# Kernel tuning notes

Hardware: AMD Instinct MI355X
Metric: run time of the kernel (lower is better)

## Reference

```python
import jax, jax.numpy as jnp
import numpy as np

N, T, D_FEAT, H = 8192, 60, 6, 64
NEG_SLOPE = 0.01  # torch LeakyReLU default


def setup_inputs() -> dict:
    key = jax.random.key(0)
    ks = jax.random.split(key, 20)
    s = lambda k, shape, fan: jax.random.normal(k, shape, jnp.float32) * (1.0 / np.sqrt(fan))
    inp = {
        'x': jax.random.normal(ks[0], (N, T, D_FEAT), jnp.float32),
        # LSTM layer 0 (input D_FEAT) and layer 1 (input H); gate order i,f,g,o
        'Wih0': s(ks[1], (4 * H, D_FEAT), H), 'Whh0': s(ks[2], (4 * H, H), H),
        'bih0': s(ks[3], (4 * H,), H), 'bhh0': s(ks[4], (4 * H,), H),
        'Wih1': s(ks[5], (4 * H, H), H), 'Whh1': s(ks[6], (4 * H, H), H),
        'bih1': s(ks[7], (4 * H,), H), 'bhh1': s(ks[8], (4 * H,), H),
        # GAT layer: transformation Linear(H,H) and attention vector a [2H,1] (randn in torch)
        'Wt': s(ks[9], (H, H), H), 'bt': s(ks[10], (H,), H),
        'a': jax.random.normal(ks[11], (2 * H, 1), jnp.float32),
        # fc and fc_out
        'Wfc': s(ks[12], (H, H), H), 'bfc': s(ks[13], (H,), H),
        'Wout': s(ks[14], (1, H), H), 'bout': s(ks[15], (1,), H),
    }
    return inp


def _lstm_layer(x, Wih, Whh, bih, bhh):
    # x: [N, T, Din] -> outputs [N, T, H]
    xg = jnp.einsum('ntd,gd->ntg', x, Wih) + bih + bhh  # precompute input gates

    def step(carry, xt):
        h, c = carry
        gates = xt + h @ Whh.T  # [N, 4H]
        i, f, g, o = jnp.split(gates, 4, axis=-1)
        c = jax.nn.sigmoid(f) * c + jax.nn.sigmoid(i) * jnp.tanh(g)
        h = jax.nn.sigmoid(o) * jnp.tanh(c)
        return (h, c), h

    n = x.shape[0]
    h0 = jnp.zeros((n, Whh.shape[1]), x.dtype)
    (_, _), hs = jax.lax.scan(step, (h0, h0), jnp.swapaxes(xg, 0, 1))
    return jnp.swapaxes(hs, 0, 1)


def _gat_layer(x, Wt, bt, a):
    # att[i,j] = leaky_relu(a1 . Wx_j + a2 . Wx_i); softmax over j; out = att @ x
    h = x @ Wt.T + bt                    # [N, H]
    hdim = h.shape[1]
    s1 = (h @ a[:hdim]).squeeze(-1)      # a1 . Wx_j  -> column term
    s2 = (h @ a[hdim:]).squeeze(-1)      # a2 . Wx_i  -> row term
    scores = jax.nn.leaky_relu(s2[:, None] + s1[None, :], NEG_SLOPE)  # [N, N]
    att = jax.nn.softmax(scores, axis=1)
    return att @ x


def reference(x, Wih0, Whh0, bih0, bhh0, Wih1, Whh1, bih1, bhh1,
              Wt, bt, a, Wfc, bfc, Wout, bout):
    out = _lstm_layer(x, Wih0, Whh0, bih0, bhh0)
    out = _lstm_layer(out, Wih1, Whh1, bih1, bhh1)
    last = out[:, -1, :]                 # [N, H]
    hidden = _gat_layer(last, Wt, bt, a) + last  # num_layers_gat = 1
    hidden = jax.nn.leaky_relu(hidden @ Wfc.T + bfc, NEG_SLOPE)
    return (hidden @ Wout.T + bout).squeeze(-1)  # [N]
```

## Files before the change

kernel.cpp:

```cpp
#include <hip/hip_runtime.h>

#define NN 8192
#define TT 60
#define DF 6
#define HH 64
#define GG 256
#define RS 132
#define CH 128
#define NCH (NN / CH)

typedef _Float16 half8 __attribute__((ext_vector_type(8)));
typedef float f32x4 __attribute__((ext_vector_type(4)));
#define MFMA16(a, b, c) __builtin_amdgcn_mfma_f32_16x16x32_f16((a), (b), (c), 0, 0, 0)

__device__ __forceinline__ float sigmoidf_(float x) {
    return __builtin_amdgcn_rcpf(1.0f + __expf(-x));
}
__device__ __forceinline__ float tanhf_(float x) {
    return __builtin_fmaf(2.0f, __builtin_amdgcn_rcpf(1.0f + __expf(-2.0f * x)), -1.0f);
}
__device__ __forceinline__ float lrelu_(float x) { return x > 0.0f ? x : 0.01f * x; }

__device__ __forceinline__ half8 ldw8(const float* __restrict__ p) {
    const float4* q = (const float4*)p;
    float4 u = q[0], v = q[1];
    half8 r;
    r[0]=(_Float16)u.x; r[1]=(_Float16)u.y; r[2]=(_Float16)u.z; r[3]=(_Float16)u.w;
    r[4]=(_Float16)v.x; r[5]=(_Float16)v.y; r[6]=(_Float16)v.z; r[7]=(_Float16)v.w;
    return r;
}

#define SXW (TT * 8 + 8)

__global__ __launch_bounds__(256, 2)
void lstm_fused_kernel(const float* __restrict__ x,
                       const float* __restrict__ Wih0, const float* __restrict__ Whh0,
                       const float* __restrict__ bih0, const float* __restrict__ bhh0,
                       const float* __restrict__ Wih1, const float* __restrict__ Whh1,
                       const float* __restrict__ bih1, const float* __restrict__ bhh1,
                       float* __restrict__ last_out)
{
    __shared__ _Float16 sxp[16][SXW];
    __shared__ _Float16 h0buf[2][16][72];
    __shared__ _Float16 h1buf[2][16][72];
    __shared__ _Float16 zero16[8];

    const int tid  = threadIdx.x;
    const int w    = tid >> 6;
    const int lane = tid & 63;
    const int quad = lane >> 4;
    const int l15  = lane & 15;
    const int hc   = w * 16 + l15;
    const int n0   = blockIdx.x * 16;

    for (int i = tid; i < 16 * SXW / 2; i += 256) ((unsigned*)sxp)[i] = 0u;
    for (int i = tid; i < 2 * 16 * 72 / 2; i += 256) ((unsigned*)h0buf)[i] = 0u;
    for (int i = tid; i < 2 * 16 * 72 / 2; i += 256) ((unsigned*)h1buf)[i] = 0u;
    if (tid < 4) ((unsigned*)zero16)[tid] = 0u;
    __syncthreads();

    for (int idx = tid; idx < 16 * TT * DF; idx += 256) {
        const int m = idx / (TT * DF);
        const int r = idx - m * (TT * DF);
        const int t = r / DF;
        const int d = r - t * DF;
        sxp[m][t * 8 + d] = (_Float16)x[(size_t)(n0 + m) * (TT * DF) + r];
    }

    half8 bhh0f[4][2], bih1f[4][2], bhh1f[4][2], bxf[4];
    float bias0[4], bias1[4];
    #pragma unroll
    for (int nt = 0; nt < 4; nt++) {
        const int g = nt * 64 + hc;
        #pragma unroll
        for (int kc = 0; kc < 2; kc++) {
            const int k0 = kc * 32 + quad * 8;
            bhh0f[nt][kc] = ldw8(Whh0 + (size_t)g * HH + k0);
            bih1f[nt][kc] = ldw8(Wih1 + (size_t)g * HH + k0);
            bhh1f[nt][kc] = ldw8(Whh1 + (size_t)g * HH + k0);
        }
        bias0[nt] = bih0[g] + bhh0[g];
        bias1[nt] = bih1[g] + bhh1[g];
        half8 t;
        #pragma unroll
        for (int j = 0; j < 8; j++) t[j] = (_Float16)0.f;
        if (quad == 0) {
            #pragma unroll
            for (int j = 0; j < DF; j++) t[j] = (_Float16)Wih0[g * DF + j];
        }
        bxf[nt] = t;
    }

    float c0[4] = {0.f, 0.f, 0.f, 0.f};
    float c1[4] = {0.f, 0.f, 0.f, 0.f};
    __syncthreads();

    int p = 0;
    for (int t = 0; t < TT; t++) {
        const half8 a_h0_0 = *(const half8*)&h0buf[p][l15][quad * 8];
        const half8 a_h0_1 = *(const half8*)&h0buf[p][l15][32 + quad * 8];
        const half8 a_h1_0 = *(const half8*)&h1buf[p][l15][quad * 8];
        const half8 a_h1_1 = *(const half8*)&h1buf[p][l15][32 + quad * 8];
        const _Float16* xap = (quad == 0) ? &sxp[l15][t * 8] : zero16;
        const half8 ax = *(const half8*)xap;

        f32x4 g0v[4];
        #pragma unroll
        for (int nt = 0; nt < 4; nt++) {
            f32x4 c; c[0] = bias0[nt]; c[1] = bias0[nt]; c[2] = bias0[nt]; c[3] = bias0[nt];
            c = MFMA16(ax, bxf[nt], c);
            c = MFMA16(a_h0_0, bhh0f[nt][0], c);
            c = MFMA16(a_h0_1, bhh0f[nt][1], c);
            g0v[nt] = c;
        }
        _Float16 (*h0w)[72] = h0buf[p ^ 1];
        #pragma unroll
        for (int reg = 0; reg < 4; reg++) {
            const float gi = g0v[0][reg], gf = g0v[1][reg], gc = g0v[2][reg], go = g0v[3][reg];
            const float cc = sigmoidf_(gf) * c0[reg] + sigmoidf_(gi) * tanhf_(gc);
            c0[reg] = cc;
            h0w[quad * 4 + reg][hc] = (_Float16)(sigmoidf_(go) * tanhf_(cc));
        }
        __syncthreads();

        const half8 a_h0n_0 = *(const half8*)&h0buf[p ^ 1][l15][quad * 8];
        const half8 a_h0n_1 = *(const half8*)&h0buf[p ^ 1][l15][32 + quad * 8];
        f32x4 g1v[4];
        #pragma unroll
        for (int nt = 0; nt < 4; nt++) {
            f32x4 c; c[0] = bias1[nt]; c[1] = bias1[nt]; c[2] = bias1[nt]; c[3] = bias1[nt];
            c = MFMA16(a_h0n_0, bih1f[nt][0], c);
            c = MFMA16(a_h0n_1, bih1f[nt][1], c);
            c = MFMA16(a_h1_0, bhh1f[nt][0], c);
            c = MFMA16(a_h1_1, bhh1f[nt][1], c);
            g1v[nt] = c;
        }
        _Float16 (*h1w)[72] = h1buf[p ^ 1];
        #pragma unroll
        for (int reg = 0; reg < 4; reg++) {
            const float gi = g1v[0][reg], gf = g1v[1][reg], gc = g1v[2][reg], go = g1v[3][reg];
            const float cc = sigmoidf_(gf) * c1[reg] + sigmoidf_(gi) * tanhf_(gc);
            c1[reg] = cc;
            const float hv = sigmoidf_(go) * tanhf_(cc);
            h1w[quad * 4 + reg][hc] = (_Float16)hv;
            if (t == TT - 1) last_out[(size_t)(n0 + quad * 4 + reg) * HH + hc] = hv;
        }
        __syncthreads();
        p ^= 1;
    }
}

__global__ void gat_prep_kernel(const float* __restrict__ last,
                                const float* __restrict__ Wt, const float* __restrict__ bt,
                                const float* __restrict__ a,
                                float* __restrict__ s1, float* __restrict__ s2,
                                float* __restrict__ blkmax)
{
    __shared__ float sWtT[HH][HH + 1];
    __shared__ float slast[16][HH];
    __shared__ float sbt[HH], sa1[HH], sa2[HH];
    __shared__ float swm[4];
    const int tid = threadIdx.x;
    for (int idx = tid; idx < HH * HH; idx += 256) {
        const int h = idx >> 6, d = idx & 63;
        sWtT[d][h] = Wt[idx];
    }
    if (tid < HH) { sbt[tid] = bt[tid]; sa1[tid] = a[tid]; sa2[tid] = a[HH + tid]; }
    const int n0 = blockIdx.x * 16;
    for (int idx = tid; idx < 16 * HH; idx += 256)
        (&slast[0][0])[idx] = last[(size_t)n0 * HH + idx];
    __syncthreads();
    const int w = tid >> 6, l = tid & 63;
    float wmax = -1e30f;
    for (int rr = 0; rr < 4; rr++) {
        const int r = w * 4 + rr;
        float acc = sbt[l];
        #pragma unroll
        for (int d = 0; d < HH; d++) acc += slast[r][d] * sWtT[d][l];
        float p1 = acc * sa1[l], p2 = acc * sa2[l];
        #pragma unroll
        for (int off = 32; off > 0; off >>= 1) {
            p1 += __shfl_xor(p1, off);
            p2 += __shfl_xor(p2, off);
        }
        if (l == 0) { s1[n0 + r] = p1; s2[n0 + r] = p2; }
        wmax = fmaxf(wmax, p1);
    }
    if (l == 0) swm[w] = wmax;
    __syncthreads();
    if (tid == 0) blkmax[blockIdx.x] = fmaxf(fmaxf(swm[0], swm[1]), fmaxf(swm[2], swm[3]));
}

__global__ void gat_finalize_kernel(const float* __restrict__ s1, const float* __restrict__ s2,
                                    const float* __restrict__ blkmax,
                                    float* __restrict__ Z, float* __restrict__ Ai, float* __restrict__ Bi,
                                    float* __restrict__ Dj, float* __restrict__ Uj, float* __restrict__ Wj,
                                    int* __restrict__ rank)
{
    __shared__ float red[256];
    const int tid = threadIdx.x;
    red[tid] = fmaxf(blkmax[tid], blkmax[tid + 256]);
    __syncthreads();
    for (int s = 128; s > 0; s >>= 1) {
        if (tid < s) red[tid] = fmaxf(red[tid], red[tid + s]);
        __syncthreads();
    }
    const float s1max = red[0];
    for (int i = blockIdx.x * 256 + tid; i < NN; i += 256 * 32) {
        const float z  = s2[i] + s1max;
        const float mi = lrelu_(z);
        Z[i]  = z;
        Ai[i] = __expf(z - mi);
        Bi[i] = __expf(0.01f * z - mi);
        const float d = s1[i] - s1max;
        Dj[i] = d;
        Uj[i] = __expf(d);
        Wj[i] = __expf(0.01f * d);
        rank[i] = 0;
    }
}

__global__ __launch_bounds__(256)
void rank_kernel(const float* __restrict__ Dj, int* __restrict__ rank)
{
    __shared__ float sd[1024];
    const int tid = threadIdx.x;
    const int j   = blockIdx.x * 256 + tid;
    const float dj = Dj[j];
    const int kbase = blockIdx.y * 1024;
    for (int i = tid; i < 1024; i += 256) sd[i] = Dj[kbase + i];
    __syncthreads();
    int cnt = 0;
    #pragma unroll 4
    for (int q = 0; q < 256; q++) {
        const float4 dk = ((const float4*)sd)[q];
        const int k0 = kbase + q * 4;
        cnt += (dk.x < dj || (dk.x == dj && k0     < j)) ? 1 : 0;
        cnt += (dk.y < dj || (dk.y == dj && k0 + 1 < j)) ? 1 : 0;
        cnt += (dk.z < dj || (dk.z == dj && k0 + 2 < j)) ? 1 : 0;
        cnt += (dk.w < dj || (dk.w == dj && k0 + 3 < j)) ? 1 : 0;
    }
    atomicAdd(&rank[j], cnt);
}

__global__ __launch_bounds__(256)
void scatter_kernel(const float* __restrict__ last,
                    const float* __restrict__ Dj, const float* __restrict__ Uj,
                    const float* __restrict__ Wj, const int* __restrict__ rank,
                    float* __restrict__ sortedRow, float* __restrict__ sortedD)
{
    const int tid = threadIdx.x;
    const int wv = tid >> 6, lane = tid & 63;
    #pragma unroll
    for (int it = 0; it < 8; it++) {
        const int j = blockIdx.x * 32 + wv * 8 + it;
        const int r = rank[j];
        const float u = Uj[j], w = Wj[j];
        const float lv = last[(size_t)j * HH + lane];
        float* row = sortedRow + (size_t)r * RS;
        row[lane]      = u * lv;
        row[64 + lane] = w * lv;
        if (lane == 0) {
            row[128] = u;
            row[129] = w;
            sortedD[r] = Dj[j];
        }
    }
}

__global__ __launch_bounds__(256)
void scanA_kernel(const float* __restrict__ sortedRow, float* __restrict__ chunkSum)
{
    const int c = threadIdx.x;
    if (c >= 130) return;
    const int b = blockIdx.x;
    const float* base = sortedRow + (size_t)b * CH * RS + c;
    float s = 0.f;
    #pragma unroll 8
    for (int r = 0; r < CH; r++) s += base[(size_t)r * RS];
    chunkSum[b * RS + c] = s;
}

__global__ __launch_bounds__(256)
void scanB_kernel(const float* __restrict__ chunkSum, float* __restrict__ chunkOfs)
{
    const int c = threadIdx.x;
    if (c >= 130) return;
    const bool rev = (c < 64) || (c == 128);
    float run = 0.f;
    if (rev) {
        for (int b = NCH - 1; b >= 0; b--) { chunkOfs[b * RS + c] = run; run += chunkSum[b * RS + c]; }
    } else {
        for (int b = 0; b < NCH; b++)      { chunkOfs[b * RS + c] = run; run += chunkSum[b * RS + c]; }
    }
}

__global__ __launch_bounds__(256)
void scanC_kernel(const float* __restrict__ sortedRow, const float* __restrict__ chunkOfs,
                  float* __restrict__ PP)
{
    const int c = threadIdx.x;
    if (c >= 130) return;
    const int b = blockIdx.x;
    const bool rev = (c < 64) || (c == 128);
    float run = chunkOfs[b * RS + c];
    if (rev) {
        if (b == NCH - 1) PP[(size_t)NN * RS + c] = 0.f;
        for (int r = CH - 1; r >= 0; r--) {
            const size_t t = (size_t)b * CH + r;
            run += sortedRow[t * RS + c];
            PP[t * RS + c] = run;
        }
    } else {
        for (int r = 0; r < CH; r++) {
            const size_t t = (size_t)b * CH + r;
            PP[t * RS + c] = run;
            run += sortedRow[t * RS + c];
        }
        if (b == NCH - 1) PP[(size_t)NN * RS + c] = run;
    }
}

__global__ __launch_bounds__(256)
void apply_kernel(const float* __restrict__ last,
                  const float* __restrict__ Z, const float* __restrict__ Ai, const float* __restrict__ Bi,
                  const float* __restrict__ sortedD, const float* __restrict__ PP,
                  float* __restrict__ gout)
{
    const int tid = threadIdx.x;
    const int wv = tid >> 6, lane = tid & 63;
    const int base_i = (blockIdx.x * 4 + wv) * 8;
    for (int batch = 0; batch < 2; batch++) {
        const int i0 = base_i + batch * 4;
        float zi[4]; int lo[4], hi[4];
        #pragma unroll
        for (int q = 0; q < 4; q++) { zi[q] = Z[i0 + q]; lo[q] = 0; hi[q] = NN; }
        for (int iter = 0; iter < 13; iter++) {
            #pragma unroll
            for (int q = 0; q < 4; q++) {
                if (lo[q] < hi[q]) {
                    const int mid = (lo[q] + hi[q]) >> 1;
                    const float dm = sortedD[mid];
                    if (zi[q] + dm > 0.f) hi[q] = mid; else lo[q] = mid + 1;
                }
            }
        }
        #pragma unroll
        for (int q = 0; q < 4; q++) {
            const int i = i0 + q;
            const int t = lo[q];
            const float ai = Ai[i], bi = Bi[i];
            const float* row = PP + (size_t)t * RS;
            const float pu  = row[lane];
            const float pw  = row[64 + lane];
            const float pud = row[128];
            const float pwd = row[129];
            const float numer = bi * pw + ai * pu;
            const float den   = bi * pwd + ai * pud;
            const float lv = last[(size_t)i * HH + lane];
            gout[(size_t)i * HH + lane] = numer * __builtin_amdgcn_rcpf(den) + lv;
        }
    }
}

__global__ void fc_out_kernel(const float* __restrict__ gout,
                              const float* __restrict__ Wfc, const float* __restrict__ bfc,
                              const float* __restrict__ Wout, const float* __restrict__ bout,
                              float* __restrict__ out)
{
    __shared__ float sW[HH][HH + 1];
    __shared__ float sb[HH], sa[HH];
    const int tid = threadIdx.x;
    for (int idx = tid; idx < HH * HH; idx += 256) {
        const int h = idx >> 6, d = idx & 63;
        sW[d][h] = Wfc[idx];
    }
    if (tid < HH) { sb[tid] = bfc[tid]; sa[tid] = Wout[tid]; }
    __syncthreads();
    const int w = tid >> 6, l = tid & 63;
    const float bo = bout[0];
    int n = blockIdx.x * 8 + w * 2;
    for (int rep = 0; rep < 2; rep++, n++) {
        const float vl = gout[(size_t)n * HH + l];
        float acc = sb[l];
        #pragma unroll
        for (int d = 0; d < HH; d++) acc += __shfl(vl, d) * sW[d][l];
        float prod = lrelu_(acc) * sa[l];
        #pragma unroll
        for (int off = 32; off > 0; off >>= 1) prod += __shfl_xor(prod, off);
        if (l == 0) out[n] = prod + bo;
    }
}

extern "C" void kernel_launch(void* const* d_in, const int* in_sizes, int n_in,
                              void* d_out, int out_size, void* d_ws, size_t ws_size,
                              hipStream_t stream)
{
    (void)in_sizes; (void)n_in; (void)out_size; (void)ws_size;
    const float* x    = (const float*)d_in[0];
    const float* Wih0 = (const float*)d_in[1];
    const float* Whh0 = (const float*)d_in[2];
    const float* bih0 = (const float*)d_in[3];
    const float* bhh0 = (const float*)d_in[4];
    const float* Wih1 = (const float*)d_in[5];
    const float* Whh1 = (const float*)d_in[6];
    const float* bih1 = (const float*)d_in[7];
    const float* bhh1 = (const float*)d_in[8];
    const float* Wt   = (const float*)d_in[9];
    const float* bt   = (const float*)d_in[10];
    const float* a    = (const float*)d_in[11];
    const float* Wfc  = (const float*)d_in[12];
    const float* bfc  = (const float*)d_in[13];
    const float* Wout = (const float*)d_in[14];
    const float* bout = (const float*)d_in[15];
    float* out = (float*)d_out;

    float* ws        = (float*)d_ws;
    float* last      = ws;
    float* gout      = last + (size_t)NN*HH;
    float* s1        = gout + (size_t)NN*HH;
    float* s2        = s1 + NN;
    float* Z         = s2 + NN;
    float* Ai        = Z + NN;
    float* Bi        = Ai + NN;
    float* Dj        = Bi + NN;
    float* Uj        = Dj + NN;
    float* Wj        = Uj + NN;
    float* blkmax    = Wj + NN;
    int*   rank      = (int*)(blkmax + 512);
    float* sortedD   = (float*)(rank + NN);
    float* sortedRow = sortedD + NN;
    float* PP        = sortedRow + (size_t)NN*RS;
    float* chunkSum  = PP + (size_t)(NN+1)*RS;
    float* chunkOfs  = chunkSum + NCH*RS;

    lstm_fused_kernel<<<dim3(NN / 16), dim3(256), 0, stream>>>(
        x, Wih0, Whh0, bih0, bhh0, Wih1, Whh1, bih1, bhh1, last);
    gat_prep_kernel<<<dim3(NN / 16), dim3(256), 0, stream>>>(
        last, Wt, bt, a, s1, s2, blkmax);
    gat_finalize_kernel<<<dim3(32), dim3(256), 0, stream>>>(
        s1, s2, blkmax, Z, Ai, Bi, Dj, Uj, Wj, rank);
    rank_kernel<<<dim3(NN / 256, 8), dim3(256), 0, stream>>>(Dj, rank);
    scatter_kernel<<<dim3(NN / 32), dim3(256), 0, stream>>>(
        last, Dj, Uj, Wj, rank, sortedRow, sortedD);
    scanA_kernel<<<dim3(NCH), dim3(256), 0, stream>>>(sortedRow, chunkSum);
    scanB_kernel<<<dim3(1), dim3(256), 0, stream>>>(chunkSum, chunkOfs);
    scanC_kernel<<<dim3(NCH), dim3(256), 0, stream>>>(sortedRow, chunkOfs, PP);
    apply_kernel<<<dim3(NN / 32), dim3(256), 0, stream>>>(
        last, Z, Ai, Bi, sortedD, PP, gout);
    fc_out_kernel<<<dim3(NN / 8), dim3(256), 0, stream>>>(
        gout, Wfc, bfc, Wout, bout, out);
}
```

Before: 287.9 us.

## Pipeline LSTM layers across wave groups, fold chunk offsets into scan, fuse apply+fc

The LSTM kernel now uses 512 threads, split into two wave groups. Layer 0 computes step i while layer 1 computes step i-1 in the same iteration, which halves the barriers per timestep and lets the two layers' MFMA work overlap. The single-block scanB kernel is removed; each scanC block now recomputes its own chunk offset by summing chunkSum directly. The apply and fc_out kernels are fused, so the gout intermediate is no longer written and reread. In exchange, the LSTM block is larger and each scanC block does redundant offset reads.

```diff
diff --git a/kernel.cpp b/kernel.cpp
--- a/kernel.cpp
+++ b/kernel.cpp
@@ -32,7 +32,7 @@
 
 #define SXW (TT * 8 + 8)
 
-__global__ __launch_bounds__(256, 2)
+__global__ __launch_bounds__(512, 4)
 void lstm_fused_kernel(const float* __restrict__ x,
                        const float* __restrict__ Wih0, const float* __restrict__ Whh0,
                        const float* __restrict__ bih0, const float* __restrict__ bhh0,
@@ -47,19 +47,21 @@
 
     const int tid  = threadIdx.x;
     const int w    = tid >> 6;
+    const int grp  = w >> 2;
+    const int cg   = w & 3;
     const int lane = tid & 63;
     const int quad = lane >> 4;
     const int l15  = lane & 15;
-    const int hc   = w * 16 + l15;
+    const int hc   = cg * 16 + l15;
     const int n0   = blockIdx.x * 16;
 
-    for (int i = tid; i < 16 * SXW / 2; i += 256) ((unsigned*)sxp)[i] = 0u;
-    for (int i = tid; i < 2 * 16 * 72 / 2; i += 256) ((unsigned*)h0buf)[i] = 0u;
-    for (int i = tid; i < 2 * 16 * 72 / 2; i += 256) ((unsigned*)h1buf)[i] = 0u;
+    for (int i = tid; i < 16 * SXW / 2; i += 512) ((unsigned*)sxp)[i] = 0u;
+    for (int i = tid; i < 2 * 16 * 72 / 2; i += 512) ((unsigned*)h0buf)[i] = 0u;
+    for (int i = tid; i < 2 * 16 * 72 / 2; i += 512) ((unsigned*)h1buf)[i] = 0u;
     if (tid < 4) ((unsigned*)zero16)[tid] = 0u;
     __syncthreads();
 
-    for (int idx = tid; idx < 16 * TT * DF; idx += 256) {
+    for (int idx = tid; idx < 16 * TT * DF; idx += 512) {
         const int m = idx / (TT * DF);
         const int r = idx - m * (TT * DF);
         const int t = r / DF;
@@ -67,86 +69,97 @@
         sxp[m][t * 8 + d] = (_Float16)x[(size_t)(n0 + m) * (TT * DF) + r];
     }
 
-    half8 bhh0f[4][2], bih1f[4][2], bhh1f[4][2], bxf[4];
-    float bias0[4], bias1[4];
+    half8 wA[4][2], wB[4][2];
+    float bias[4];
+    half8 hzero;
     #pragma unroll
-    for (int nt = 0; nt < 4; nt++) {
-        const int g = nt * 64 + hc;
-        #pragma unroll
-        for (int kc = 0; kc < 2; kc++) {
-            const int k0 = kc * 32 + quad * 8;
-            bhh0f[nt][kc] = ldw8(Whh0 + (size_t)g * HH + k0);
-            bih1f[nt][kc] = ldw8(Wih1 + (size_t)g * HH + k0);
-            bhh1f[nt][kc] = ldw8(Whh1 + (size_t)g * HH + k0);
-        }
-        bias0[nt] = bih0[g] + bhh0[g];
-        bias1[nt] = bih1[g] + bhh1[g];
-        half8 t;
-        #pragma unroll
-        for (int j = 0; j < 8; j++) t[j] = (_Float16)0.f;
-        if (quad == 0) {
-            #pragma unroll
-            for (int j = 0; j < DF; j++) t[j] = (_Float16)Wih0[g * DF + j];
-        }
-        bxf[nt] = t;
-    }
-
-    float c0[4] = {0.f, 0.f, 0.f, 0.f};
-    float c1[4] = {0.f, 0.f, 0.f, 0.f};
-    __syncthreads();
-
-    int p = 0;
-    for (int t = 0; t < TT; t++) {
-        const half8 a_h0_0 = *(const half8*)&h0buf[p][l15][quad * 8];
-        const half8 a_h0_1 = *(const half8*)&h0buf[p][l15][32 + quad * 8];
-        const half8 a_h1_0 = *(const half8*)&h1buf[p][l15][quad * 8];
-        const half8 a_h1_1 = *(const half8*)&h1buf[p][l15][32 + quad * 8];
-        const _Float16* xap = (quad == 0) ? &sxp[l15][t * 8] : zero16;
-        const half8 ax = *(const half8*)xap;
-
-        f32x4 g0v[4];
+    for (int j = 0; j < 8; j++) hzero[j] = (_Float16)0.f;
+
+    if (grp == 0) {
         #pragma unroll
         for (int nt = 0; nt < 4; nt++) {
-            f32x4 c; c[0] = bias0[nt]; c[1] = bias0[nt]; c[2] = bias0[nt]; c[3] = bias0[nt];
-            c = MFMA16(ax, bxf[nt], c);
-            c = MFMA16(a_h0_0, bhh0f[nt][0], c);
-            c = MFMA16(a_h0_1, bhh0f[nt][1], c);
-            g0v[nt] = c;
-        }
-        _Float16 (*h0w)[72] = h0buf[p ^ 1];
-        #pragma unroll
-        for (int reg = 0; reg < 4; reg++) {
-            const float gi = g0v[0][reg], gf = g0v[1][reg], gc = g0v[2][reg], go = g0v[3][reg];
-            const float cc = sigmoidf_(gf) * c0[reg] + sigmoidf_(gi) * tanhf_(gc);
-            c0[reg] = cc;
-            h0w[quad * 4 + reg][hc] = (_Float16)(sigmoidf_(go) * tanhf_(cc));
+            const int g = nt * 64 + hc;
+            wA[nt][0] = ldw8(Whh0 + (size_t)g * HH + quad * 8);
+            wA[nt][1] = ldw8(Whh0 + (size_t)g * HH + 32 + quad * 8);
+            bias[nt]  = bih0[g] + bhh0[g];
+            half8 t = hzero;
+            if (quad == 0) {
+                #pragma unroll
+                for (int j = 0; j < DF; j++) t[j] = (_Float16)Wih0[g * DF + j];
+            }
+            wB[nt][0] = t;
+            wB[nt][1] = hzero;
+        }
+    } else {
+        #pragma unroll
+        for (int nt = 0; nt < 4; nt++) {
+            const int g = nt * 64 + hc;
+            wA[nt][0] = ldw8(Wih1 + (size_t)g * HH + quad * 8);
+            wA[nt][1] = ldw8(Wih1 + (size_t)g * HH + 32 + quad * 8);
+            wB[nt][0] = ldw8(Whh1 + (size_t)g * HH + quad * 8);
+            wB[nt][1] = ldw8(Whh1 + (size_t)g * HH + 32 + quad * 8);
+            bias[nt]  = bih1[g] + bhh1[g];
+        }
+    }
+
+    float cs[4] = {0.f, 0.f, 0.f, 0.f};
+    __syncthreads();
+
+    for (int i = 0; i <= TT; i++) {
+        const int p = i & 1;
+        if (grp == 0) {
+            if (i < TT) {
+                const half8 a0 = *(const half8*)&h0buf[p][l15][quad * 8];
+                const half8 a1 = *(const half8*)&h0buf[p][l15][32 + quad * 8];
+                const _Float16* xap = (quad == 0) ? &sxp[l15][i * 8] : zero16;
+                const half8 ax = *(const half8*)xap;
+                f32x4 gv[4];
+                #pragma unroll
+                for (int nt = 0; nt < 4; nt++) {
+                    f32x4 c; c[0] = bias[nt]; c[1] = bias[nt]; c[2] = bias[nt]; c[3] = bias[nt];
+                    c = MFMA16(ax, wB[nt][0], c);
+                    c = MFMA16(a0, wA[nt][0], c);
+                    c = MFMA16(a1, wA[nt][1], c);
+                    gv[nt] = c;
+                }
+                _Float16 (*h0w)[72] = h0buf[p ^ 1];
+                #pragma unroll
+                for (int reg = 0; reg < 4; reg++) {
+                    const float gi = gv[0][reg], gf = gv[1][reg], gc = gv[2][reg], go = gv[3][reg];
+                    const float cc = sigmoidf_(gf) * cs[reg] + sigmoidf_(gi) * tanhf_(gc);
+                    cs[reg] = cc;
+                    h0w[quad * 4 + reg][hc] = (_Float16)(sigmoidf_(go) * tanhf_(cc));
+                }
+            }
+        } else {
+            if (i > 0) {
+                const half8 a00 = *(const half8*)&h0buf[p][l15][quad * 8];
+                const half8 a01 = *(const half8*)&h0buf[p][l15][32 + quad * 8];
+                const half8 a10 = *(const half8*)&h1buf[p][l15][quad * 8];
+                const half8 a11 = *(const half8*)&h1buf[p][l15][32 + quad * 8];
+                f32x4 gv[4];
+                #pragma unroll
+                for (int nt = 0; nt < 4; nt++) {
+                    f32x4 c; c[0] = bias[nt]; c[1] = bias[nt]; c[2] = bias[nt]; c[3] = bias[nt];
+                    c = MFMA16(a00, wA[nt][0], c);
+                    c = MFMA16(a01, wA[nt][1], c);
+                    c = MFMA16(a10, wB[nt][0], c);
+                    c = MFMA16(a11, wB[nt][1], c);
+                    gv[nt] = c;
+                }
+                _Float16 (*h1w)[72] = h1buf[p ^ 1];
+                #pragma unroll
+                for (int reg = 0; reg < 4; reg++) {
+                    const float gi = gv[0][reg], gf = gv[1][reg], gc = gv[2][reg], go = gv[3][reg];
+                    const float cc = sigmoidf_(gf) * cs[reg] + sigmoidf_(gi) * tanhf_(gc);
+                    cs[reg] = cc;
+                    const float hv = sigmoidf_(go) * tanhf_(cc);
+                    h1w[quad * 4 + reg][hc] = (_Float16)hv;
+                    if (i == TT) last_out[(size_t)(n0 + quad * 4 + reg) * HH + hc] = hv;
+                }
+            }
         }
         __syncthreads();
-
-        const half8 a_h0n_0 = *(const half8*)&h0buf[p ^ 1][l15][quad * 8];
-        const half8 a_h0n_1 = *(const half8*)&h0buf[p ^ 1][l15][32 + quad * 8];
-        f32x4 g1v[4];
-        #pragma unroll
-        for (int nt = 0; nt < 4; nt++) {
-            f32x4 c; c[0] = bias1[nt]; c[1] = bias1[nt]; c[2] = bias1[nt]; c[3] = bias1[nt];
-            c = MFMA16(a_h0n_0, bih1f[nt][0], c);
-            c = MFMA16(a_h0n_1, bih1f[nt][1], c);
-            c = MFMA16(a_h1_0, bhh1f[nt][0], c);
-            c = MFMA16(a_h1_1, bhh1f[nt][1], c);
-            g1v[nt] = c;
-        }
-        _Float16 (*h1w)[72] = h1buf[p ^ 1];
-        #pragma unroll
-        for (int reg = 0; reg < 4; reg++) {
-            const float gi = g1v[0][reg], gf = g1v[1][reg], gc = g1v[2][reg], go = g1v[3][reg];
-            const float cc = sigmoidf_(gf) * c1[reg] + sigmoidf_(gi) * tanhf_(gc);
-            c1[reg] = cc;
-            const float hv = sigmoidf_(go) * tanhf_(cc);
-            h1w[quad * 4 + reg][hc] = (_Float16)hv;
-            if (t == TT - 1) last_out[(size_t)(n0 + quad * 4 + reg) * HH + hc] = hv;
-        }
-        __syncthreads();
-        p ^= 1;
     }
 }
 
@@ -282,36 +295,30 @@
 }
 
 __global__ __launch_bounds__(256)
-void scanB_kernel(const float* __restrict__ chunkSum, float* __restrict__ chunkOfs)
-{
-    const int c = threadIdx.x;
-    if (c >= 130) return;
-    const bool rev = (c < 64) || (c == 128);
-    float run = 0.f;
-    if (rev) {
-        for (int b = NCH - 1; b >= 0; b--) { chunkOfs[b * RS + c] = run; run += chunkSum[b * RS + c]; }
-    } else {
-        for (int b = 0; b < NCH; b++)      { chunkOfs[b * RS + c] = run; run += chunkSum[b * RS + c]; }
-    }
-}
-
-__global__ __launch_bounds__(256)
-void scanC_kernel(const float* __restrict__ sortedRow, const float* __restrict__ chunkOfs,
+void scanC_kernel(const float* __restrict__ sortedRow, const float* __restrict__ chunkSum,
                   float* __restrict__ PP)
 {
     const int c = threadIdx.x;
     if (c >= 130) return;
     const int b = blockIdx.x;
     const bool rev = (c < 64) || (c == 128);
-    float run = chunkOfs[b * RS + c];
+    float run = 0.f;
+    #pragma unroll 8
+    for (int bb = 0; bb < NCH; bb++) {
+        const float v = chunkSum[bb * RS + c];
+        const bool take = rev ? (bb > b) : (bb < b);
+        run += take ? v : 0.f;
+    }
     if (rev) {
         if (b == NCH - 1) PP[(size_t)NN * RS + c] = 0.f;
+        #pragma unroll 4
         for (int r = CH - 1; r >= 0; r--) {
             const size_t t = (size_t)b * CH + r;
             run += sortedRow[t * RS + c];
             PP[t * RS + c] = run;
         }
     } else {
+        #pragma unroll 4
         for (int r = 0; r < CH; r++) {
             const size_t t = (size_t)b * CH + r;
             PP[t * RS + c] = run;
@@ -322,14 +329,26 @@
 }
 
 __global__ __launch_bounds__(256)
-void apply_kernel(const float* __restrict__ last,
-                  const float* __restrict__ Z, const float* __restrict__ Ai, const float* __restrict__ Bi,
-                  const float* __restrict__ sortedD, const float* __restrict__ PP,
-                  float* __restrict__ gout)
-{
+void applyfc_kernel(const float* __restrict__ last,
+                    const float* __restrict__ Z, const float* __restrict__ Ai, const float* __restrict__ Bi,
+                    const float* __restrict__ sortedD, const float* __restrict__ PP,
+                    const float* __restrict__ Wfc, const float* __restrict__ bfc,
+                    const float* __restrict__ Wout, const float* __restrict__ bout,
+                    float* __restrict__ out)
+{
+    __shared__ float sW[HH][HH + 1];
+    __shared__ float sb[HH], sa[HH];
     const int tid = threadIdx.x;
+    for (int idx = tid; idx < HH * HH; idx += 256) {
+        const int h = idx >> 6, d = idx & 63;
+        sW[d][h] = Wfc[idx];
+    }
+    if (tid < HH) { sb[tid] = bfc[tid]; sa[tid] = Wout[tid]; }
+    __syncthreads();
+
     const int wv = tid >> 6, lane = tid & 63;
     const int base_i = (blockIdx.x * 4 + wv) * 8;
+    const float bo = bout[0];
     for (int batch = 0; batch < 2; batch++) {
         const int i0 = base_i + batch * 4;
         float zi[4]; int lo[4], hi[4];
@@ -358,37 +377,15 @@
             const float numer = bi * pw + ai * pu;
             const float den   = bi * pwd + ai * pud;
             const float lv = last[(size_t)i * HH + lane];
-            gout[(size_t)i * HH + lane] = numer * __builtin_amdgcn_rcpf(den) + lv;
-        }
-    }
-}
-
-__global__ void fc_out_kernel(const float* __restrict__ gout,
-                              const float* __restrict__ Wfc, const float* __restrict__ bfc,
-                              const float* __restrict__ Wout, const float* __restrict__ bout,
-                              float* __restrict__ out)
-{
-    __shared__ float sW[HH][HH + 1];
-    __shared__ float sb[HH], sa[HH];
-    const int tid = threadIdx.x;
-    for (int idx = tid; idx < HH * HH; idx += 256) {
-        const int h = idx >> 6, d = idx & 63;
-        sW[d][h] = Wfc[idx];
-    }
-    if (tid < HH) { sb[tid] = bfc[tid]; sa[tid] = Wout[tid]; }
-    __syncthreads();
-    const int w = tid >> 6, l = tid & 63;
-    const float bo = bout[0];
-    int n = blockIdx.x * 8 + w * 2;
-    for (int rep = 0; rep < 2; rep++, n++) {
-        const float vl = gout[(size_t)n * HH + l];
-        float acc = sb[l];
-        #pragma unroll
-        for (int d = 0; d < HH; d++) acc += __shfl(vl, d) * sW[d][l];
-        float prod = lrelu_(acc) * sa[l];
-        #pragma unroll
-        for (int off = 32; off > 0; off >>= 1) prod += __shfl_xor(prod, off);
-        if (l == 0) out[n] = prod + bo;
+            const float gv = numer * __builtin_amdgcn_rcpf(den) + lv;
+            float acc = sb[lane];
+            #pragma unroll
+            for (int d = 0; d < HH; d++) acc += __shfl(gv, d) * sW[d][lane];
+            float prod = lrelu_(acc) * sa[lane];
+            #pragma unroll
+            for (int off = 32; off > 0; off >>= 1) prod += __shfl_xor(prod, off);
+            if (lane == 0) out[i] = prod + bo;
+        }
     }
 }
 
@@ -417,8 +414,7 @@
 
     float* ws        = (float*)d_ws;
     float* last      = ws;
-    float* gout      = last + (size_t)NN*HH;
-    float* s1        = gout + (size_t)NN*HH;
+    float* s1        = last + (size_t)NN*HH;
     float* s2        = s1 + NN;
     float* Z         = s2 + NN;
     float* Ai        = Z + NN;
@@ -432,9 +428,8 @@
     float* sortedRow = sortedD + NN;
     float* PP        = sortedRow + (size_t)NN*RS;
     float* chunkSum  = PP + (size_t)(NN+1)*RS;
-    float* chunkOfs  = chunkSum + NCH*RS;
-
-    lstm_fused_kernel<<<dim3(NN / 16), dim3(256), 0, stream>>>(
+
+    lstm_fused_kernel<<<dim3(NN / 16), dim3(512), 0, stream>>>(
         x, Wih0, Whh0, bih0, bhh0, Wih1, Whh1, bih1, bhh1, last);
     gat_prep_kernel<<<dim3(NN / 16), dim3(256), 0, stream>>>(
         last, Wt, bt, a, s1, s2, blkmax);
@@ -444,10 +439,7 @@
     scatter_kernel<<<dim3(NN / 32), dim3(256), 0, stream>>>(
         last, Dj, Uj, Wj, rank, sortedRow, sortedD);
     scanA_kernel<<<dim3(NCH), dim3(256), 0, stream>>>(sortedRow, chunkSum);
-    scanB_kernel<<<dim3(1), dim3(256), 0, stream>>>(chunkSum, chunkOfs);
-    scanC_kernel<<<dim3(NCH), dim3(256), 0, stream>>>(sortedRow, chunkOfs, PP);
-    apply_kernel<<<dim3(NN / 32), dim3(256), 0, stream>>>(
-        last, Z, Ai, Bi, sortedD, PP, gout);
-    fc_out_kernel<<<dim3(NN / 8), dim3(256), 0, stream>>>(
-        gout, Wfc, bfc, Wout, bout, out);
-}
+    scanC_kernel<<<dim3(NCH), dim3(256), 0, stream>>>(sortedRow, chunkSum, PP);
+    applyfc_kernel<<<dim3(NN / 32), dim3(256), 0, stream>>>(
+        last, Z, Ai, Bi, sortedD, PP, Wfc, bfc, Wout, bout, out);
+}
```

Measured after the change: 292.4 us. About the same (+1.5%).
